# Kernel tuning notes

Measured on AMD Instinct MI355X. Metric: run time of the kernel, lower is better.

The kernel has to match this reference:

```python
import jax, jax.numpy as jnp
import numpy as np

N_NODES = 100000
N_EDGES = 3200000
H, D = 3, 12  # heads, per-head dim; H*D == node_hidden_dim == 36
NEG_SLOPE = 0.2


def setup_inputs() -> dict:
    key = jax.random.key(0)
    ks = jax.random.split(key, 11)
    s = 0.1
    return {
        "node_features": jax.random.normal(ks[0], (N_NODES, 36), jnp.float32),
        "src": jax.random.randint(ks[1], (N_EDGES,), 0, N_NODES),
        "dst": jax.random.randint(ks[2], (N_EDGES,), 0, N_NODES),
        "lin0_w": jax.random.normal(ks[3], (36, 36), jnp.float32) * s,
        "lin0_b": jax.random.normal(ks[4], (36,), jnp.float32) * s,
        "fc_w": jax.random.normal(ks[5], (3, 36, 36), jnp.float32) * s,
        "attn_l": jax.random.normal(ks[6], (3, H, D), jnp.float32) * s,
        "attn_r": jax.random.normal(ks[7], (3, H, D), jnp.float32) * s,
        "gat_bias": jax.random.normal(ks[8], (3, 36), jnp.float32) * s,
        "out_w": jax.random.normal(ks[9], (36, 36), jnp.float32) * s,
        "out_b": jax.random.normal(ks[10], (36,), jnp.float32) * s,
    }


def _gat_layer(h, src, dst, fc_w, a_l, a_r, bias):
    n = h.shape[0]
    feat = (h @ fc_w).reshape(n, H, D)                      # (N,H,D)
    el = jnp.sum(feat * a_l, axis=-1)                       # (N,H)
    er = jnp.sum(feat * a_r, axis=-1)                       # (N,H)
    e = el[src] + er[dst]                                   # (E,H)
    e = jnp.where(e >= 0, e, NEG_SLOPE * e)                 # leaky_relu(0.2)
    # edge softmax over incoming edges of each dst node (numerically stable)
    m = jax.ops.segment_max(e, dst, num_segments=n)         # (N,H)
    m = jnp.where(jnp.isfinite(m), m, 0.0)                  # zero-degree guard
    ee = jnp.exp(e - m[dst])                                # (E,H)
    denom = jax.ops.segment_sum(ee, dst, num_segments=n)    # (N,H)
    alpha = ee / jnp.maximum(denom[dst], 1e-9)              # (E,H)
    msg = feat[src] * alpha[:, :, None]                     # (E,H,D)
    rst = jax.ops.segment_sum(msg, dst, num_segments=n)     # (N,H,D)
    # residual (Identity since in_feats == H*D) + bias, then ELU
    rst = rst + h.reshape(n, H, D) + bias.reshape(1, H, D)
    return jax.nn.elu(rst).reshape(n, H * D)


def reference(node_features, src, dst, lin0_w, lin0_b, fc_w, attn_l, attn_r, gat_bias, out_w, out_b):
    h = node_features @ lin0_w + lin0_b
    for l in range(3):
        h = _gat_layer(h, src, dst, fc_w[l], attn_l[l], attn_r[l], gat_bias[l])
    return h @ out_w + out_b
```

## Files before the change

### kernel.cpp

```cpp
#include <hip/hip_runtime.h>
#include <math.h>

#define HID 36
#define NH 3
#define HD 12
#define PROW 64
#define BSHIFT 13
#define NBUCK 13
#define PSHIFT 8
#define PCHUNK 2048
#define SPCAP 9216
#define CSRCAP 4096
#define NSTEP 8

typedef _Float16 f16;


__global__ void __launch_bounds__(192)
lin0_hist_kernel(const float* __restrict__ x, const float* __restrict__ w0,
                 const float* __restrict__ b0, const float* __restrict__ fcw,
                 const float* __restrict__ al, const float* __restrict__ ar,
                 float* __restrict__ h, f16* __restrict__ packed,
                 float* __restrict__ er, int n, int nb_lin,
                 const int* __restrict__ dst, int* __restrict__ M, int E, int C,
                 int np) {
    int t = threadIdx.x;
    if ((int)blockIdx.x >= nb_lin) {
        __shared__ int hcnt[512];
        int c = blockIdx.x - nb_lin;
        for (int i = t; i < 512; i += 192) hcnt[i] = 0;
        __syncthreads();
        int i0 = c * PCHUNK;
        int i1 = min(i0 + PCHUNK, E);
        for (int i = i0 + t; i < i1; i += 192)
            atomicAdd(&hcnt[dst[i] >> PSHIFT], 1);
        __syncthreads();
        for (int b = t; b < np; b += 192)
            M[(size_t)b * C + c] = hcnt[b];
        return;
    }
    __shared__ float W0[HID * HID];
    __shared__ float W1[HID * HID];
    __shared__ float Bs[HID], ALs[HID], ARs[HID];
    __shared__ float xsh[64 * 37];
    __shared__ float hsh[64 * 37];
    for (int i = t; i < HID * HID; i += 192) { W0[i] = w0[i]; W1[i] = fcw[i]; }
    if (t < HID) { Bs[t] = b0[t]; ALs[t] = al[t]; ARs[t] = ar[t]; }
    int nb0 = blockIdx.x * 64;
    int nrow = min(64, n - nb0);
    for (int i = t; i < nrow * HID; i += 192) {
        int r = i / HID, cc = i - r * HID;
        xsh[r * 37 + cc] = x[(size_t)nb0 * HID + i];
        (void)cc;
    }
    __syncthreads();
    int ln = t / 3, hh = t - ln * 3;
    int node = nb0 + ln;
    bool active = (node < n);

    float h0s[HD];
#pragma unroll
    for (int d = 0; d < HD; ++d) h0s[d] = Bs[hh * HD + d];
    const float* xrow = &xsh[ln * 37];
#pragma unroll 4
    for (int k = 0; k < HID; ++k) {
        float xv = xrow[k];
        const float* w = &W0[k * HID + hh * HD];
#pragma unroll
        for (int d = 0; d < HD; ++d) h0s[d] += xv * w[d];
    }
    if (active) {
        float4* hp = (float4*)(h + (size_t)node * HID + hh * HD);
        hp[0] = make_float4(h0s[0], h0s[1], h0s[2], h0s[3]);
        hp[1] = make_float4(h0s[4], h0s[5], h0s[6], h0s[7]);
        hp[2] = make_float4(h0s[8], h0s[9], h0s[10], h0s[11]);
    }
#pragma unroll
    for (int d = 0; d < HD; ++d) hsh[ln * 37 + hh * HD + d] = h0s[d];
    __syncthreads();

    float feat[HD];
#pragma unroll
    for (int d = 0; d < HD; ++d) feat[d] = 0.f;
    const float* hrow = &hsh[ln * 37];
#pragma unroll 4
    for (int k = 0; k < HID; ++k) {
        float hv = hrow[k];
        const float* w = &W1[k * HID + hh * HD];
#pragma unroll
        for (int d = 0; d < HD; ++d) feat[d] += hv * w[d];
    }
    if (!active) return;
    float sl = 0.f, sr = 0.f;
#pragma unroll
    for (int d = 0; d < HD; ++d) {
        sl += feat[d] * ALs[hh * HD + d];
        sr += feat[d] * ARs[hh * HD + d];
    }
    union { f16 hx[16]; uint4 q[2]; } o;
#pragma unroll
    for (int d = 0; d < HD; ++d) o.hx[d] = (f16)feat[d];
    o.hx[12] = (f16)sl;
    o.hx[13] = (f16)0.f; o.hx[14] = (f16)0.f; o.hx[15] = (f16)0.f;
    uint4* prow = (uint4*)(packed + (size_t)node * PROW + hh * 16);
    prow[0] = o.q[0];
    prow[1] = o.q[1];
    er[node * NH + hh] = sr;
}

__global__ void base_scan_kernel(const int* __restrict__ M, int* __restrict__ BaseT,
                                 int* __restrict__ T, int C, int np) {
    __shared__ int tmp[512];
    int b = blockIdx.x;
    int t = threadIdx.x;
    int carry = 0;
    for (int base = 0; base < C; base += 512) {
        int idx = base + t;
        int v = (idx < C) ? M[(size_t)b * C + idx] : 0;
        tmp[t] = v;
        __syncthreads();
        for (int ofs = 1; ofs < 512; ofs <<= 1) {
            int x = 0;
            if (t >= ofs) x = tmp[t - ofs];
            __syncthreads();
            tmp[t] += x;
            __syncthreads();
        }
        if (idx < C) BaseT[(size_t)idx * 512 + b] = carry + tmp[t] - v;
        carry += tmp[511];
        __syncthreads();
    }
    if (t == 0) T[b] = carry;
}

__global__ void part_scatter_kernel(const int* __restrict__ src, const int* __restrict__ dst,
                                    const int* __restrict__ BaseT, const int* __restrict__ T,
                                    int* __restrict__ part, int E, int np) {
    __shared__ int tsc[512];
    __shared__ int base[512];
    __shared__ int hexcl[512];
    __shared__ int hcur[512];
    __shared__ int smsrc[PCHUNK];
    __shared__ int smdst[PCHUNK];
    __shared__ int smsort[PCHUNK];
    __shared__ short smbin[PCHUNK];
    int t = threadIdx.x;
    int c = blockIdx.x;
    int v = (t < np) ? T[t] : 0;
    tsc[t] = v;
    hcur[t] = 0;
    __syncthreads();
    for (int ofs = 1; ofs < 512; ofs <<= 1) {
        int x = 0;
        if (t >= ofs) x = tsc[t - ofs];
        __syncthreads();
        tsc[t] += x;
        __syncthreads();
    }
    if (t < np) base[t] = (tsc[t] - v) + BaseT[(size_t)c * 512 + t];
    __syncthreads();
    int i0 = c * PCHUNK;
    int cnum = min(i0 + PCHUNK, E) - i0;
    for (int i = t; i < cnum; i += 512) {
        int s = src[i0 + i], d = dst[i0 + i];
        smsrc[i] = s;
        smdst[i] = d;
        atomicAdd(&hcur[d >> PSHIFT], 1);
    }
    __syncthreads();
    int hv = hcur[t];
    tsc[t] = hv;
    __syncthreads();
    for (int ofs = 1; ofs < 512; ofs <<= 1) {
        int x = 0;
        if (t >= ofs) x = tsc[t - ofs];
        __syncthreads();
        tsc[t] += x;
        __syncthreads();
    }
    hexcl[t] = tsc[t] - hv;
    hcur[t] = tsc[t] - hv;
    __syncthreads();
    for (int i = t; i < cnum; i += 512) {
        int d = smdst[i];
        int bin = d >> PSHIFT;
        int pos = atomicAdd(&hcur[bin], 1);
        smsort[pos] = (smsrc[i] << PSHIFT) | (d & ((1 << PSHIFT) - 1));
        smbin[pos] = (short)bin;
    }
    __syncthreads();
    for (int i = t; i < cnum; i += 512) {
        int bin = smbin[i];
        part[base[bin] + (i - hexcl[bin])] = smsort[i];
    }
}

__global__ void bucket_csr_kernel(const int* __restrict__ part, const int* __restrict__ T,
                                  int* __restrict__ csr, int* __restrict__ off,
                                  int n, int E, int np) {
    __shared__ int cnt[256 * NBUCK];
    __shared__ int psum[512];
    __shared__ int smout[SPCAP];
    __shared__ int e0s;
    int p = blockIdx.x;
    int t = threadIdx.x;
    int v = (t < np) ? T[t] : 0;
    psum[t] = v;
    __syncthreads();
    for (int ofs = 1; ofs < 512; ofs <<= 1) {
        int x = 0;
        if (t >= ofs) x = psum[t - ofs];
        __syncthreads();
        psum[t] += x;
        __syncthreads();
    }
    if (t == p) e0s = psum[t] - v;
    __syncthreads();
    int e0 = e0s;
    int dbase = p << PSHIFT;
    int nd = min(256, n - dbase);
    int nc = nd * NBUCK;
    for (int i = t; i < nc; i += blockDim.x) cnt[i] = 0;
    __syncthreads();
    int cnt_p = T[p];
    const int* pp = part + e0;
    bool fits = (cnt_p <= SPCAP);
    for (int i = t; i < cnt_p; i += blockDim.x) {
        int e = pp[i];
        atomicAdd(&cnt[(e & 255) * NBUCK + ((e >> PSHIFT) >> BSHIFT)], 1);
    }
    __syncthreads();
    int sum = 0;
    if (t < nd) {
        for (int k = 0; k < NBUCK; ++k) {
            int c = cnt[t * NBUCK + k];
            cnt[t * NBUCK + k] = sum;
            sum += c;
        }
    }
    psum[t] = (t < nd) ? sum : 0;
    __syncthreads();
    for (int ofs = 1; ofs < 512; ofs <<= 1) {
        int x = 0;
        if (t >= ofs) x = psum[t - ofs];
        __syncthreads();
        psum[t] += x;
        __syncthreads();
    }
    int dexcl = (t > 0) ? psum[t - 1] : 0;
    int start = e0 + dexcl;
    if (t < nd) {
        for (int k = 0; k < NBUCK; ++k) cnt[t * NBUCK + k] += start;
        off[dbase + t] = start;
    }
    __syncthreads();
    if (fits) {
        for (int i = t; i < cnt_p; i += blockDim.x) {
            int e = pp[i];
            int s = e >> PSHIFT;
            int idx = (e & 255) * NBUCK + (s >> BSHIFT);
            int pos = atomicAdd(&cnt[idx], 1);
            smout[pos - e0] = s << 6;
        }
        __syncthreads();
        for (int i = t; i < cnt_p; i += blockDim.x)
            csr[e0 + i] = smout[i];
    } else {
        for (int i = t; i < cnt_p; i += blockDim.x) {
            int e = pp[i];
            int s = e >> PSHIFT;
            int idx = (e & 255) * NBUCK + (s >> BSHIFT);
            int pos = atomicAdd(&cnt[idx], 1);
            csr[pos] = s << 6;
        }
    }
    if (p == 0 && t == 0) off[n] = E;
}


__device__ __forceinline__ void edge_accum(uint4 qa, uint4 qb, float ern,
                                           float& denom, float* acc) {
    union { uint4 q[2]; f16 hx[16]; } v;
    v.q[0] = qa;
    v.q[1] = qb;
    float e = (float)v.hx[12] + ern;
    e = (e >= 0.f) ? e : 0.2f * e;
    float w = __expf(e);
    denom += w;
#pragma unroll
    for (int k = 0; k < HD; ++k) acc[k] += w * (float)v.hx[k];
}

template <bool FITS>
__device__ __forceinline__ void sweep_paced(const int* __restrict__ smbuf,
                                            const int* __restrict__ csre,
                                            int j0, int deg, const f16* __restrict__ pb,
                                            float ern, float& denom, float* acc) {
    int j = j0;
#pragma unroll 1
    for (int s2 = 1; s2 <= NSTEP; ++s2) {
        int jend = j0 + ((deg * s2) >> 3);
        int c = jend - j;
        for (; c >= 4; c -= 4, j += 4) {
            int o0 = FITS ? smbuf[j]     : csre[j];
            int o1 = FITS ? smbuf[j + 1] : csre[j + 1];
            int o2 = FITS ? smbuf[j + 2] : csre[j + 2];
            int o3 = FITS ? smbuf[j + 3] : csre[j + 3];
            const uint4* r0 = (const uint4*)(pb + o0);
            const uint4* r1 = (const uint4*)(pb + o1);
            const uint4* r2 = (const uint4*)(pb + o2);
            const uint4* r3 = (const uint4*)(pb + o3);
            uint4 a0 = r0[0], b0 = r0[1];
            uint4 a1 = r1[0], b1 = r1[1];
            uint4 a2 = r2[0], b2 = r2[1];
            uint4 a3 = r3[0], b3 = r3[1];
            edge_accum(a0, b0, ern, denom, acc);
            edge_accum(a1, b1, ern, denom, acc);
            edge_accum(a2, b2, ern, denom, acc);
            edge_accum(a3, b3, ern, denom, acc);
        }
        for (; c > 0; --c, ++j) {
            int o = FITS ? smbuf[j] : csre[j];
            const uint4* r = (const uint4*)(pb + o);
            edge_accum(r[0], r[1], ern, denom, acc);
        }
    }
}

__global__ void __launch_bounds__(192)
aggtr_kernel(const f16* __restrict__ packed_in, const float* __restrict__ er_in,
             const float* __restrict__ hcur,
             const int* __restrict__ off, const int* __restrict__ csr,
             const float* __restrict__ bias, const float* __restrict__ wnext,
             const float* __restrict__ aln, const float* __restrict__ arn,
             float* __restrict__ hnext, f16* __restrict__ packed_out,
             float* __restrict__ er_out, int n) {
    __shared__ float Wsh[HID * HID];
    __shared__ float ALs[HID], ARs[HID];
    __shared__ int smbuf[CSRCAP];
    int t = threadIdx.x;
    for (int i = t; i < HID * HID; i += 192) Wsh[i] = wnext[i];
    if (t < HID) { ALs[t] = aln[t]; ARs[t] = arn[t]; }
    int ln = t / 3, hh = t - ln * 3;
    int nb0 = blockIdx.x * 64;
    int node = nb0 + ln;
    bool active = (node < n);

    int e0 = off[nb0];
    int e1 = off[min(nb0 + 64, n)];
    int span = e1 - e0;
    bool fits = (span <= CSRCAP);
    if (fits)
        for (int i = t; i < span; i += 192) smbuf[i] = csr[e0 + i];

    int j0 = 0, deg = 0;
    float ern = 0.f;
    if (active) {
        j0 = off[node] - e0;
        deg = off[node + 1] - e0 - j0;
        ern = er_in[node * NH + hh];
    }
    const f16* pb = packed_in + hh * 16;
    const int* csre = csr + e0;
    __syncthreads();

    float denom = 0.f;
    float acc[HD];
#pragma unroll
    for (int k = 0; k < HD; ++k) acc[k] = 0.f;

    if (fits) sweep_paced<true>(smbuf, csre, j0, deg, pb, ern, denom, acc);
    else      sweep_paced<false>(smbuf, csre, j0, deg, pb, ern, denom, acc);
    __syncthreads();

    float* hsh = (float*)smbuf;
    float v[HD];
#pragma unroll
    for (int k = 0; k < HD; ++k) v[k] = 0.f;
    if (active) {
        float inv = 1.f / fmaxf(denom, 1e-9f);
        int base = node * HID + hh * HD;
        const float4* hc = (const float4*)(hcur + base);
        float4 h0 = hc[0], h1 = hc[1], h2 = hc[2];
        float hres[HD] = {h0.x, h0.y, h0.z, h0.w, h1.x, h1.y, h1.z, h1.w, h2.x, h2.y, h2.z, h2.w};
#pragma unroll
        for (int k = 0; k < HD; ++k) {
            float x = acc[k] * inv + hres[k] + bias[hh * HD + k];
            v[k] = (x > 0.f) ? x : expm1f(x);
        }
        float4* hp = (float4*)(hnext + base);
        hp[0] = make_float4(v[0], v[1], v[2], v[3]);
        hp[1] = make_float4(v[4], v[5], v[6], v[7]);
        hp[2] = make_float4(v[8], v[9], v[10], v[11]);
    }
#pragma unroll
    for (int k = 0; k < HD; ++k) hsh[ln * 37 + hh * HD + k] = v[k];
    __syncthreads();

    float feat[HD];
#pragma unroll
    for (int d = 0; d < HD; ++d) feat[d] = 0.f;
    const float* hrow = &hsh[ln * 37];
#pragma unroll 4
    for (int k = 0; k < HID; ++k) {
        float hv = hrow[k];
        const float* w = &Wsh[k * HID + hh * HD];
#pragma unroll
        for (int d = 0; d < HD; ++d) feat[d] += hv * w[d];
    }
    if (!active) return;
    float sl = 0.f, sr = 0.f;
#pragma unroll
    for (int d = 0; d < HD; ++d) {
        sl += feat[d] * ALs[hh * HD + d];
        sr += feat[d] * ARs[hh * HD + d];
    }
    union { f16 hx[16]; uint4 q[2]; } o;
#pragma unroll
    for (int d = 0; d < HD; ++d) o.hx[d] = (f16)feat[d];
    o.hx[12] = (f16)sl;
    o.hx[13] = (f16)0.f; o.hx[14] = (f16)0.f; o.hx[15] = (f16)0.f;
    uint4* prow = (uint4*)(packed_out + (size_t)node * PROW + hh * 16);
    prow[0] = o.q[0];
    prow[1] = o.q[1];
    er_out[node * NH + hh] = sr;
}

__global__ void __launch_bounds__(192)
aggout_kernel(const f16* __restrict__ packed_in, const float* __restrict__ er_in,
              const float* __restrict__ hcur,
              const int* __restrict__ off, const int* __restrict__ csr,
              const float* __restrict__ bias, const float* __restrict__ ow,
              const float* __restrict__ ob, float* __restrict__ out, int n) {
    __shared__ float Wsh[HID * HID];
    __shared__ float OBs[HID];
    __shared__ int smbuf[CSRCAP];
    int t = threadIdx.x;
    for (int i = t; i < HID * HID; i += 192) Wsh[i] = ow[i];
    if (t < HID) OBs[t] = ob[t];
    int ln = t / 3, hh = t - ln * 3;
    int nb0 = blockIdx.x * 64;
    int node = nb0 + ln;
    bool active = (node < n);

    int e0 = off[nb0];
    int e1 = off[min(nb0 + 64, n)];
    int span = e1 - e0;
    bool fits = (span <= CSRCAP);
    if (fits)
        for (int i = t; i < span; i += 192) smbuf[i] = csr[e0 + i];

    int j0 = 0, deg = 0;
    float ern = 0.f;
    if (active) {
        j0 = off[node] - e0;
        deg = off[node + 1] - e0 - j0;
        ern = er_in[node * NH + hh];
    }
    const f16* pb = packed_in + hh * 16;
    const int* csre = csr + e0;
    __syncthreads();

    float denom = 0.f;
    float acc[HD];
#pragma unroll
    for (int k = 0; k < HD; ++k) acc[k] = 0.f;

    if (fits) sweep_paced<true>(smbuf, csre, j0, deg, pb, ern, denom, acc);
    else      sweep_paced<false>(smbuf, csre, j0, deg, pb, ern, denom, acc);
    __syncthreads();

    float* hsh = (float*)smbuf;
    float v[HD];
#pragma unroll
    for (int k = 0; k < HD; ++k) v[k] = 0.f;
    if (active) {
        float inv = 1.f / fmaxf(denom, 1e-9f);
        int base = node * HID + hh * HD;
        const float4* hc = (const float4*)(hcur + base);
        float4 h0 = hc[0], h1 = hc[1], h2 = hc[2];
        float hres[HD] = {h0.x, h0.y, h0.z, h0.w, h1.x, h1.y, h1.z, h1.w, h2.x, h2.y, h2.z, h2.w};
#pragma unroll
        for (int k = 0; k < HD; ++k) {
            float x = acc[k] * inv + hres[k] + bias[hh * HD + k];
            v[k] = (x > 0.f) ? x : expm1f(x);
        }
    }
#pragma unroll
    for (int k = 0; k < HD; ++k) hsh[ln * 37 + hh * HD + k] = v[k];
    __syncthreads();

    float feat[HD];
#pragma unroll
    for (int d = 0; d < HD; ++d) feat[d] = OBs[hh * HD + d];
    const float* hrow = &hsh[ln * 37];
#pragma unroll 4
    for (int k = 0; k < HID; ++k) {
        float hv = hrow[k];
        const float* w = &Wsh[k * HID + hh * HD];
#pragma unroll
        for (int d = 0; d < HD; ++d) feat[d] += hv * w[d];
    }
    if (!active) return;
    float4* op = (float4*)(out + (size_t)node * HID + hh * HD);
    op[0] = make_float4(feat[0], feat[1], feat[2], feat[3]);
    op[1] = make_float4(feat[4], feat[5], feat[6], feat[7]);
    op[2] = make_float4(feat[8], feat[9], feat[10], feat[11]);
}


extern "C" void kernel_launch(void* const* d_in, const int* in_sizes, int n_in,
                              void* d_out, int out_size, void* d_ws, size_t ws_size,
                              hipStream_t stream) {
    const float* xnf = (const float*)d_in[0];
    const int* src = (const int*)d_in[1];
    const int* dst = (const int*)d_in[2];
    const float* l0w = (const float*)d_in[3];
    const float* l0b = (const float*)d_in[4];
    const float* fcw = (const float*)d_in[5];
    const float* al  = (const float*)d_in[6];
    const float* ar  = (const float*)d_in[7];
    const float* gb  = (const float*)d_in[8];
    const float* ow  = (const float*)d_in[9];
    const float* ob  = (const float*)d_in[10];
    float* out = (float*)d_out;
    const int N = in_sizes[0] / HID;
    const int E = in_sizes[1];
    const int NP = (N + (1 << PSHIFT) - 1) >> PSHIFT;
    const int C = (E + PCHUNK - 1) / PCHUNK;

    char* p = (char*)d_ws;
    auto alloc = [&](size_t bytes) {
        char* r = p;
        p += (bytes + 255) & ~(size_t)255;
        return r;
    };
    int* part    = (int*)alloc((size_t)E * 4);
    int* M       = (int*)alloc((size_t)NP * C * 4);
    int* BaseT   = (int*)alloc((size_t)C * 512 * 4);
    int* T       = (int*)alloc((size_t)NP * 4);
    int* off     = (int*)alloc((size_t)(N + 1) * 4);
    int* csr     = (int*)alloc((size_t)E * 4);
    float* ha    = (float*)alloc((size_t)N * HID * 4);
    float* hb    = (float*)alloc((size_t)N * HID * 4);
    f16* pkA     = (f16*)alloc((size_t)N * PROW * 2);
    f16* pkB     = (f16*)alloc((size_t)N * PROW * 2);
    float* erA   = (float*)alloc((size_t)N * NH * 4);
    float* erB   = (float*)alloc((size_t)N * NH * 4);

    int nblk_lin = (N + 63) / 64;
    int fblk = (N + 63) / 64;

    lin0_hist_kernel<<<nblk_lin + C, 192, 0, stream>>>(xnf, l0w, l0b, fcw, al, ar,
                                                       ha, pkA, erA, N, nblk_lin,
                                                       dst, M, E, C, NP);
    base_scan_kernel<<<NP, 512, 0, stream>>>(M, BaseT, T, C, NP);
    part_scatter_kernel<<<C, 512, 0, stream>>>(src, dst, BaseT, T, part, E, NP);
    bucket_csr_kernel<<<NP, 512, 0, stream>>>(part, T, csr, off, N, E, NP);

    aggtr_kernel<<<fblk, 192, 0, stream>>>(pkA, erA, ha, off, csr, gb,
                                           fcw + (size_t)1 * HID * HID, al + HID, ar + HID,
                                           hb, pkB, erB, N);
    aggtr_kernel<<<fblk, 192, 0, stream>>>(pkB, erB, hb, off, csr, gb + HID,
                                           fcw + (size_t)2 * HID * HID, al + 2 * HID, ar + 2 * HID,
                                           ha, pkA, erA, N);
    aggout_kernel<<<fblk, 192, 0, stream>>>(pkA, erA, ha, off, csr, gb + 2 * HID,
                                            ow, ob, out, N);
}
```

Before: 336.6 us.

## Replace global partition scatter with per-chunk local sort and per-bucket segment gathering

```diff
diff --git a/kernel.cpp b/kernel.cpp
--- a/kernel.cpp
+++ b/kernel.cpp
@@ -9,6 +9,7 @@
 #define NBUCK 13
 #define PSHIFT 8
 #define PCHUNK 2048
+#define NPAD 400
 #define SPCAP 9216
 #define CSRCAP 4096
 #define NSTEP 8
@@ -17,33 +18,17 @@
 
 
 __global__ void __launch_bounds__(192)
-lin0_hist_kernel(const float* __restrict__ x, const float* __restrict__ w0,
-                 const float* __restrict__ b0, const float* __restrict__ fcw,
-                 const float* __restrict__ al, const float* __restrict__ ar,
-                 float* __restrict__ h, f16* __restrict__ packed,
-                 float* __restrict__ er, int n, int nb_lin,
-                 const int* __restrict__ dst, int* __restrict__ M, int E, int C,
-                 int np) {
-    int t = threadIdx.x;
-    if ((int)blockIdx.x >= nb_lin) {
-        __shared__ int hcnt[512];
-        int c = blockIdx.x - nb_lin;
-        for (int i = t; i < 512; i += 192) hcnt[i] = 0;
-        __syncthreads();
-        int i0 = c * PCHUNK;
-        int i1 = min(i0 + PCHUNK, E);
-        for (int i = i0 + t; i < i1; i += 192)
-            atomicAdd(&hcnt[dst[i] >> PSHIFT], 1);
-        __syncthreads();
-        for (int b = t; b < np; b += 192)
-            M[(size_t)b * C + c] = hcnt[b];
-        return;
-    }
+lin0_kernel(const float* __restrict__ x, const float* __restrict__ w0,
+            const float* __restrict__ b0, const float* __restrict__ fcw,
+            const float* __restrict__ al, const float* __restrict__ ar,
+            float* __restrict__ h, f16* __restrict__ packed,
+            float* __restrict__ er, int n) {
     __shared__ float W0[HID * HID];
     __shared__ float W1[HID * HID];
     __shared__ float Bs[HID], ALs[HID], ARs[HID];
     __shared__ float xsh[64 * 37];
     __shared__ float hsh[64 * 37];
+    int t = threadIdx.x;
     for (int i = t; i < HID * HID; i += 192) { W0[i] = w0[i]; W1[i] = fcw[i]; }
     if (t < HID) { Bs[t] = b0[t]; ALs[t] = al[t]; ARs[t] = ar[t]; }
     int nb0 = blockIdx.x * 64;
@@ -51,7 +36,6 @@
     for (int i = t; i < nrow * HID; i += 192) {
         int r = i / HID, cc = i - r * HID;
         xsh[r * 37 + cc] = x[(size_t)nb0 * HID + i];
-        (void)cc;
     }
     __syncthreads();
     int ln = t / 3, hh = t - ln * 3;
@@ -108,56 +92,19 @@
     er[node * NH + hh] = sr;
 }
 
-__global__ void base_scan_kernel(const int* __restrict__ M, int* __restrict__ BaseT,
-                                 int* __restrict__ T, int C, int np) {
-    __shared__ int tmp[512];
-    int b = blockIdx.x;
-    int t = threadIdx.x;
-    int carry = 0;
-    for (int base = 0; base < C; base += 512) {
-        int idx = base + t;
-        int v = (idx < C) ? M[(size_t)b * C + idx] : 0;
-        tmp[t] = v;
-        __syncthreads();
-        for (int ofs = 1; ofs < 512; ofs <<= 1) {
-            int x = 0;
-            if (t >= ofs) x = tmp[t - ofs];
-            __syncthreads();
-            tmp[t] += x;
-            __syncthreads();
-        }
-        if (idx < C) BaseT[(size_t)idx * 512 + b] = carry + tmp[t] - v;
-        carry += tmp[511];
-        __syncthreads();
-    }
-    if (t == 0) T[b] = carry;
-}
-
-__global__ void part_scatter_kernel(const int* __restrict__ src, const int* __restrict__ dst,
-                                    const int* __restrict__ BaseT, const int* __restrict__ T,
-                                    int* __restrict__ part, int E, int np) {
-    __shared__ int tsc[512];
-    __shared__ int base[512];
+__global__ void histsort_kernel(const int* __restrict__ src, const int* __restrict__ dst,
+                                int* __restrict__ part, int* __restrict__ Mscan,
+                                int* __restrict__ Mcnt, int E, int C, int np) {
+    __shared__ int hcnt[512];
     __shared__ int hexcl[512];
     __shared__ int hcur[512];
+    __shared__ int tsc[512];
     __shared__ int smsrc[PCHUNK];
     __shared__ int smdst[PCHUNK];
     __shared__ int smsort[PCHUNK];
-    __shared__ short smbin[PCHUNK];
     int t = threadIdx.x;
     int c = blockIdx.x;
-    int v = (t < np) ? T[t] : 0;
-    tsc[t] = v;
-    hcur[t] = 0;
-    __syncthreads();
-    for (int ofs = 1; ofs < 512; ofs <<= 1) {
-        int x = 0;
-        if (t >= ofs) x = tsc[t - ofs];
-        __syncthreads();
-        tsc[t] += x;
-        __syncthreads();
-    }
-    if (t < np) base[t] = (tsc[t] - v) + BaseT[(size_t)c * 512 + t];
+    hcnt[t] = 0;
     __syncthreads();
     int i0 = c * PCHUNK;
     int cnum = min(i0 + PCHUNK, E) - i0;
@@ -165,10 +112,10 @@
         int s = src[i0 + i], d = dst[i0 + i];
         smsrc[i] = s;
         smdst[i] = d;
-        atomicAdd(&hcur[d >> PSHIFT], 1);
-    }
-    __syncthreads();
-    int hv = hcur[t];
+        atomicAdd(&hcnt[d >> PSHIFT], 1);
+    }
+    __syncthreads();
+    int hv = hcnt[t];
     tsc[t] = hv;
     __syncthreads();
     for (int ofs = 1; ofs < 512; ofs <<= 1) {
@@ -183,21 +130,37 @@
     __syncthreads();
     for (int i = t; i < cnum; i += 512) {
         int d = smdst[i];
-        int bin = d >> PSHIFT;
-        int pos = atomicAdd(&hcur[bin], 1);
+        int pos = atomicAdd(&hcur[d >> PSHIFT], 1);
         smsort[pos] = (smsrc[i] << PSHIFT) | (d & ((1 << PSHIFT) - 1));
-        smbin[pos] = (short)bin;
-    }
-    __syncthreads();
-    for (int i = t; i < cnum; i += 512) {
-        int bin = smbin[i];
-        part[base[bin] + (i - hexcl[bin])] = smsort[i];
-    }
-}
-
-__global__ void bucket_csr_kernel(const int* __restrict__ part, const int* __restrict__ T,
+    }
+    __syncthreads();
+    for (int i = t; i < cnum; i += 512)
+        part[(size_t)c * PCHUNK + i] = smsort[i];
+    if (t < np) {
+        Mscan[(size_t)c * NPAD + t] = hexcl[t];
+        Mcnt[(size_t)c * NPAD + t] = hcur[t] - hexcl[t];
+    }
+}
+
+__global__ void colsum_kernel(const int* __restrict__ Mcnt, int* __restrict__ T,
+                              int C, int np) {
+    __shared__ int red[512];
+    int b = blockIdx.x, t = threadIdx.x;
+    int s = 0;
+    for (int c = t; c < C; c += 512) s += Mcnt[(size_t)c * NPAD + b];
+    red[t] = s;
+    __syncthreads();
+    for (int ofs = 256; ofs > 0; ofs >>= 1) {
+        if (t < ofs) red[t] += red[t + ofs];
+        __syncthreads();
+    }
+    if (t == 0) T[b] = red[0];
+}
+
+__global__ void bucket_csr_kernel(const int* __restrict__ part, const int* __restrict__ Mscan,
+                                  const int* __restrict__ Mcnt, const int* __restrict__ T,
                                   int* __restrict__ csr, int* __restrict__ off,
-                                  int n, int E, int np) {
+                                  int n, int E, int C, int np) {
     __shared__ int cnt[256 * NBUCK];
     __shared__ int psum[512];
     __shared__ int smout[SPCAP];
@@ -217,17 +180,25 @@
     if (t == p) e0s = psum[t] - v;
     __syncthreads();
     int e0 = e0s;
+    int cnt_p = T[p];
     int dbase = p << PSHIFT;
     int nd = min(256, n - dbase);
     int nc = nd * NBUCK;
-    for (int i = t; i < nc; i += blockDim.x) cnt[i] = 0;
-    __syncthreads();
-    int cnt_p = T[p];
-    const int* pp = part + e0;
+    for (int i = t; i < nc; i += 512) cnt[i] = 0;
+    __syncthreads();
     bool fits = (cnt_p <= SPCAP);
-    for (int i = t; i < cnt_p; i += blockDim.x) {
-        int e = pp[i];
-        atomicAdd(&cnt[(e & 255) * NBUCK + ((e >> PSHIFT) >> BSHIFT)], 1);
+    for (int cb = 0; cb < C; cb += 512) {
+        int c = cb + t;
+        int cc = 0;
+        size_t sstart = 0;
+        if (c < C) {
+            cc = Mcnt[(size_t)c * NPAD + p];
+            sstart = (size_t)c * PCHUNK + Mscan[(size_t)c * NPAD + p];
+        }
+        for (int k = 0; k < cc; ++k) {
+            int e = part[sstart + k];
+            atomicAdd(&cnt[(e & 255) * NBUCK + ((e >> PSHIFT) >> BSHIFT)], 1);
+        }
     }
     __syncthreads();
     int sum = 0;
@@ -255,23 +226,41 @@
     }
     __syncthreads();
     if (fits) {
-        for (int i = t; i < cnt_p; i += blockDim.x) {
-            int e = pp[i];
-            int s = e >> PSHIFT;
-            int idx = (e & 255) * NBUCK + (s >> BSHIFT);
-            int pos = atomicAdd(&cnt[idx], 1);
-            smout[pos - e0] = s << 6;
-        }
-        __syncthreads();
-        for (int i = t; i < cnt_p; i += blockDim.x)
+        for (int cb = 0; cb < C; cb += 512) {
+            int c = cb + t;
+            int cc = 0;
+            size_t sstart = 0;
+            if (c < C) {
+                cc = Mcnt[(size_t)c * NPAD + p];
+                sstart = (size_t)c * PCHUNK + Mscan[(size_t)c * NPAD + p];
+            }
+            for (int k = 0; k < cc; ++k) {
+                int e = part[sstart + k];
+                int s = e >> PSHIFT;
+                int idx = (e & 255) * NBUCK + (s >> BSHIFT);
+                int pos = atomicAdd(&cnt[idx], 1);
+                smout[pos - e0] = s << 6;
+            }
+        }
+        __syncthreads();
+        for (int i = t; i < cnt_p; i += 512)
             csr[e0 + i] = smout[i];
     } else {
-        for (int i = t; i < cnt_p; i += blockDim.x) {
-            int e = pp[i];
-            int s = e >> PSHIFT;
-            int idx = (e & 255) * NBUCK + (s >> BSHIFT);
-            int pos = atomicAdd(&cnt[idx], 1);
-            csr[pos] = s << 6;
+        for (int cb = 0; cb < C; cb += 512) {
+            int c = cb + t;
+            int cc = 0;
+            size_t sstart = 0;
+            if (c < C) {
+                cc = Mcnt[(size_t)c * NPAD + p];
+                sstart = (size_t)c * PCHUNK + Mscan[(size_t)c * NPAD + p];
+            }
+            for (int k = 0; k < cc; ++k) {
+                int e = part[sstart + k];
+                int s = e >> PSHIFT;
+                int idx = (e & 255) * NBUCK + (s >> BSHIFT);
+                int pos = atomicAdd(&cnt[idx], 1);
+                csr[pos] = s << 6;
+            }
         }
     }
     if (p == 0 && t == 0) off[n] = E;
@@ -535,9 +524,9 @@
         p += (bytes + 255) & ~(size_t)255;
         return r;
     };
-    int* part    = (int*)alloc((size_t)E * 4);
-    int* M       = (int*)alloc((size_t)NP * C * 4);
-    int* BaseT   = (int*)alloc((size_t)C * 512 * 4);
+    int* part    = (int*)alloc((size_t)C * PCHUNK * 4);
+    int* Mscan   = (int*)alloc((size_t)C * NPAD * 4);
+    int* Mcnt    = (int*)alloc((size_t)C * NPAD * 4);
     int* T       = (int*)alloc((size_t)NP * 4);
     int* off     = (int*)alloc((size_t)(N + 1) * 4);
     int* csr     = (int*)alloc((size_t)E * 4);
@@ -551,12 +540,12 @@
     int nblk_lin = (N + 63) / 64;
     int fblk = (N + 63) / 64;
 
-    lin0_hist_kernel<<<nblk_lin + C, 192, 0, stream>>>(xnf, l0w, l0b, fcw, al, ar,
-                                                       ha, pkA, erA, N, nblk_lin,
-                                                       dst, M, E, C, NP);
-    base_scan_kernel<<<NP, 512, 0, stream>>>(M, BaseT, T, C, NP);
-    part_scatter_kernel<<<C, 512, 0, stream>>>(src, dst, BaseT, T, part, E, NP);
-    bucket_csr_kernel<<<NP, 512, 0, stream>>>(part, T, csr, off, N, E, NP);
+    lin0_kernel<<<nblk_lin, 192, 0, stream>>>(xnf, l0w, l0b, fcw, al, ar,
+                                              ha, pkA, erA, N);
+    histsort_kernel<<<C, 512, 0, stream>>>(src, dst, part, Mscan, Mcnt, E, C, NP);
+    colsum_kernel<<<NP, 512, 0, stream>>>(Mcnt, T, C, NP);
+    bucket_csr_kernel<<<NP, 512, 0, stream>>>(part, Mscan, Mcnt, T, csr, off,
+                                              N, E, C, NP);
 
     aggtr_kernel<<<fblk, 192, 0, stream>>>(pkA, erA, ha, off, csr, gb,
                                            fcw + (size_t)1 * HID * HID, al + HID, ar + HID,
```

Result: slower. 360.8 us (+7.2%).
